# Kernel optimization log

Measured on AMD Instinct MI355X. Metric: run time of the kernel, lower is better.

The kernel has to match this reference:

```python
import jax, jax.numpy as jnp
import numpy as np

K = 20
EPS = 1e-5
SLOPE = 0.2


def _knn_idx(x, k):
    # x: [B, C, N] -> idx [B, N, k] of nearest neighbors by squared L2
    sq = jnp.sum(x * x, axis=1)                      # [B, N]
    inner = jnp.einsum('bcn,bcm->bnm', x, x)         # [B, N, N]
    neg_dist = 2.0 * inner - sq[:, :, None] - sq[:, None, :]
    return jax.lax.top_k(neg_dist, k)[1]             # [B, N, k]


def _edge_block(x, W, gamma, beta, k):
    # x: [B, C, N]; W: [O, 2C]; returns [B, O, N]
    idx = _knn_idx(x, k)
    xt = jnp.transpose(x, (0, 2, 1))                 # [B, N, C]
    nb = jax.vmap(lambda t, i: t[i])(xt, idx)        # [B, N, k, C] gather
    ctr = xt[:, :, None, :]
    edge = jnp.concatenate(
        [nb - ctr, jnp.broadcast_to(ctr, nb.shape)], axis=-1)  # [B, N, k, 2C]
    y = jnp.einsum('bnkc,oc->bonk', edge, W)         # 1x1 conv
    # BatchNorm2d (training mode: batch stats over B,N,k per channel)
    m = jnp.mean(y, axis=(0, 2, 3), keepdims=True)
    v = jnp.var(y, axis=(0, 2, 3), keepdims=True)
    y = (y - m) * jax.lax.rsqrt(v + EPS)
    y = y * gamma[None, :, None, None] + beta[None, :, None, None]
    y = jnp.where(y >= 0, y, SLOPE * y)              # LeakyReLU(0.2)
    return jnp.max(y, axis=-1)                       # max over k neighbors


def setup_inputs() -> dict:
    key = jax.random.key(0)
    ks = jax.random.split(key, 8)
    B, N = 8, 2048
    x = jax.random.normal(ks[0], (B, N, 3), dtype=jnp.float32)
    W1 = jax.random.normal(ks[1], (64, 6), dtype=jnp.float32) * 0.2
    W2 = jax.random.normal(ks[2], (128, 128), dtype=jnp.float32) * 0.08
    W3 = jax.random.normal(ks[3], (256, 256), dtype=jnp.float32) * 0.06
    g1, b1 = jnp.ones((64,), jnp.float32), jnp.zeros((64,), jnp.float32)
    g2, b2 = jnp.ones((128,), jnp.float32), jnp.zeros((128,), jnp.float32)
    g3, b3 = jnp.ones((256,), jnp.float32), jnp.zeros((256,), jnp.float32)
    L1 = jax.random.normal(ks[4], (1024, 448), dtype=jnp.float32) * 0.04
    L2 = jax.random.normal(ks[5], (2500, 1024), dtype=jnp.float32) * 0.03
    return {"x": x, "W1": W1, "g1": g1, "b1": b1, "W2": W2, "g2": g2,
            "b2": b2, "W3": W3, "g3": g3, "b3": b3, "L1": L1, "L2": L2}


def reference(x, W1, g1, b1, W2, g2, b2, W3, g3, b3, L1, L2):
    xT = jnp.transpose(x, (0, 2, 1))                 # [B, 3, N]
    x1 = _edge_block(xT, W1, g1, b1, K)              # [B, 64, N]
    x2 = _edge_block(x1, W2, g2, b2, K)              # [B, 128, N]
    x3 = _edge_block(x2, W3, g3, b3, K)              # [B, 256, N]
    feat = jnp.concatenate([x1, x2, x3], axis=1)     # [B, 448, N]
    pooled = jnp.max(feat, axis=-1)                  # adaptive_max_pool1d(1)
    h = pooled @ L1.T
    h = jnp.where(h >= 0, h, SLOPE * h)              # LeakyReLU(0.2)
    # dropout is identity in eval mode
    return h @ L2.T                                  # [B, 2500]
```

## Files before the change

### kernel.cpp

```cpp
#include <hip/hip_runtime.h>
#include <hip/hip_bf16.h>
#include <float.h>

#define K_NN 20
#define EPS 1e-5f
#define SLOPE 0.2f
constexpr int Bsz = 8;
constexpr int Npts = 2048;
constexpr int NQ = 8;
constexpr int BN = Bsz * Npts;

typedef __attribute__((ext_vector_type(8))) short short8v;
typedef __attribute__((ext_vector_type(4))) float f32x4;

__device__ __forceinline__ float dot4(float4 a, float4 b) {
  return a.x*b.x + a.y*b.y + a.z*b.z + a.w*b.w;
}
__device__ __forceinline__ unsigned encf(float f) {
  unsigned u = __float_as_uint(f);
  return (u & 0x80000000u) ? ~u : (u | 0x80000000u);
}
__device__ __forceinline__ float decf(unsigned e) {
  unsigned u = (e & 0x80000000u) ? (e & 0x7fffffffu) : ~e;
  return __uint_as_float(u);
}
__device__ __forceinline__ unsigned short f2bf(float x) {
  unsigned u = __float_as_uint(x);
  unsigned r = (u + 0x7fffu + ((u >> 16) & 1u)) >> 16;
  return (unsigned short)r;
}
__device__ __forceinline__ float bf2f(unsigned short h) {
  return __uint_as_float((unsigned)h << 16);
}
__device__ __forceinline__ f32x4 mfma16(short8v a, short8v b, f32x4 c) {
  return __builtin_amdgcn_mfma_f32_16x16x32_bf16(a, b, c, 0, 0, 0);
}

template<int C>
__global__ __launch_bounds__(256) void sq_kernel(const float* __restrict__ xt,
                                                 float* __restrict__ sq) {
  int p = blockIdx.x * 256 + threadIdx.x;
  if (p >= BN) return;
  const float* r = xt + (size_t)p * C;
  float s = 0.f;
  if constexpr (C % 4 == 0) {
    for (int c4 = 0; c4 < C / 4; ++c4) { float4 v = *(const float4*)(r + c4 * 4); s += dot4(v, v); }
  } else {
    #pragma unroll
    for (int c = 0; c < C; ++c) { float v = r[c]; s += v * v; }
  }
  sq[p] = s;
}

template<int C, int MT>
__global__ __launch_bounds__(256) void knn_part(const float* __restrict__ xt,
    const float* __restrict__ sq, float* __restrict__ pval, int* __restrict__ pidx) {
  constexpr int MQ = Npts / NQ;
  __shared__ __align__(16) float chk[MT][C];
  __shared__ float csq[MT];
  const int t = threadIdx.x, w = t >> 6, l = t & 63;
  const int rowblk = blockIdx.x / NQ;
  const int q = blockIdx.x - rowblk * NQ;
  const int p0 = rowblk * 256;
  const int b = p0 / Npts;
  const int myrow = p0 + w * 64 + l;

  float cr[C];
  #pragma unroll
  for (int c = 0; c < C; ++c) cr[c] = xt[(size_t)myrow * C + c];
  const float sqn = sq[myrow];

  float vals[K_NN]; int ids[K_NN];
  #pragma unroll
  for (int i = 0; i < K_NN; ++i) { vals[i] = -FLT_MAX; ids[i] = 0; }

  const int mbase = q * MQ;
  for (int m0 = mbase; m0 < mbase + MQ; m0 += MT) {
    __syncthreads();
    const float* s2 = xt + ((size_t)b * Npts + m0) * C;
    for (int e = t; e < MT * C; e += 256) chk[e / C][e - (e / C) * C] = s2[e];
    for (int e = t; e < MT; e += 256) csq[e] = sq[b * Npts + m0 + e];
    __syncthreads();
    for (int j = 0; j < MT; ++j) {
      float dt = 0.f;
      #pragma unroll
      for (int c = 0; c < C; ++c) dt += cr[c] * chk[j][c];
      float nd = 2.f * dt - sqn - csq[j];
      if (nd > vals[K_NN - 1]) {
        vals[K_NN - 1] = nd; ids[K_NN - 1] = m0 + j;
        #pragma unroll
        for (int i = K_NN - 1; i >= 1; --i) {
          if (vals[i] > vals[i - 1]) {
            float tv = vals[i]; vals[i] = vals[i-1]; vals[i-1] = tv;
            int ti = ids[i]; ids[i] = ids[i-1]; ids[i-1] = ti;
          }
        }
      }
    }
  }
  size_t base = ((size_t)q * BN + myrow) * K_NN;
  #pragma unroll
  for (int i = 0; i < K_NN; ++i) { pval[base + i] = vals[i]; pidx[base + i] = ids[i]; }
}

__global__ __launch_bounds__(256) void knn_merge(const float* __restrict__ pval,
    const int* __restrict__ pidx, int* __restrict__ idxout) {
  int p = blockIdx.x * 256 + threadIdx.x;
  if (p >= BN) return;
  float vals[K_NN]; int ids[K_NN];
  size_t base = (size_t)p * K_NN;
  #pragma unroll
  for (int i = 0; i < K_NN; ++i) { vals[i] = pval[base + i]; ids[i] = pidx[base + i]; }
  for (int q = 1; q < NQ; ++q) {
    size_t b2 = ((size_t)q * BN + p) * K_NN;
    #pragma unroll
    for (int i = 0; i < K_NN; ++i) {
      float v = pval[b2 + i];
      if (v <= vals[K_NN - 1]) break;
      int m = pidx[b2 + i];
      vals[K_NN - 1] = v; ids[K_NN - 1] = m;
      #pragma unroll
      for (int r = K_NN - 1; r >= 1; --r) {
        if (vals[r] > vals[r - 1]) {
          float tv = vals[r]; vals[r] = vals[r-1]; vals[r-1] = tv;
          int ti = ids[r]; ids[r] = ids[r-1]; ids[r-1] = ti;
        }
      }
    }
  }
  int* op = idxout + (size_t)p * K_NN;
  #pragma unroll
  for (int i = 0; i < K_NN; ++i) op[i] = ids[i];
}

template<int C>
__global__ __launch_bounds__(256) void knn_fused(
    const unsigned short* __restrict__ xh, const unsigned short* __restrict__ xl,
    const float* __restrict__ sq, int* __restrict__ idxout) {
  constexpr int KS = C / 32;
  constexpr int TPW = Npts / 64 / 4;
  __shared__ float dist[4][64][17];
  __shared__ float svv[4][16][K_NN];
  __shared__ int   sii[4][16][K_NN];
  const int b = blockIdx.x >> 7, qt = blockIdx.x & 127;
  const int q0 = qt * 16;
  const int t = threadIdx.x, wv = t >> 6, l = t & 63, l15 = l & 15, grp = l >> 4;
  const unsigned short* xbh = xh + (size_t)b * Npts * C;
  const unsigned short* xbl = xl + (size_t)b * Npts * C;
  const float* sqb = sq + b * Npts;
  const int qi = q0 + l15;

  short8v bh[KS], bl[KS];
  #pragma unroll
  for (int ks = 0; ks < KS; ++ks) {
    const size_t a = (size_t)qi * C + ks * 32 + grp * 8;
    bh[ks] = *(const short8v*)(xbh + a);
    bl[ks] = *(const short8v*)(xbl + a);
  }
  const float sqn = sqb[qi];

  float vals[K_NN]; int ids[K_NN];
  #pragma unroll
  for (int i = 0; i < K_NN; ++i) { vals[i] = -FLT_MAX; ids[i] = 0; }

  #pragma unroll 1
  for (int ti = 0; ti < TPW; ++ti) {
    const int m0 = (wv * TPW + ti) * 64;
    f32x4 acc[4];
    #pragma unroll
    for (int rt = 0; rt < 4; ++rt) acc[rt] = (f32x4){0.f, 0.f, 0.f, 0.f};
    #pragma unroll
    for (int ks = 0; ks < KS; ++ks) {
      #pragma unroll
      for (int rt = 0; rt < 4; ++rt) {
        const size_t aoff = (size_t)(m0 + rt * 16 + l15) * C + ks * 32 + grp * 8;
        const short8v a_h = *(const short8v*)(xbh + aoff);
        const short8v a_l = *(const short8v*)(xbl + aoff);
        acc[rt] = mfma16(a_h, bh[ks], acc[rt]);
        acc[rt] = mfma16(a_l, bh[ks], acc[rt]);
        acc[rt] = mfma16(a_h, bl[ks], acc[rt]);
      }
    }
    #pragma unroll
    for (int rt = 0; rt < 4; ++rt) {
      const int cb = m0 + rt * 16 + grp * 4;
      const float4 s4 = *(const float4*)(sqb + cb);
      const float sv[4] = {s4.x, s4.y, s4.z, s4.w};
      #pragma unroll
      for (int r = 0; r < 4; ++r) {
        const int cand = cb + r;
        float v = 2.f * acc[rt][r] - sqn - sv[r];
        if (cand == qi) v = 0.f;
        dist[wv][rt * 16 + grp * 4 + r][l15] = v;
      }
    }
    asm volatile("s_waitcnt lgkmcnt(0)" ::: "memory");
    __builtin_amdgcn_sched_barrier(0);
    #pragma unroll 1
    for (int j = 0; j < 16; ++j) {
      const float v = dist[wv][grp * 16 + j][l15];
      if (v > vals[K_NN - 1]) {
        const int cand = m0 + grp * 16 + j;
        vals[K_NN - 1] = v; ids[K_NN - 1] = cand;
        #pragma unroll
        for (int i = K_NN - 1; i >= 1; --i) {
          if (vals[i] > vals[i - 1]) {
            float tv = vals[i]; vals[i] = vals[i-1]; vals[i-1] = tv;
            int ti2 = ids[i]; ids[i] = ids[i-1]; ids[i-1] = ti2;
          }
        }
      }
    }
  }

  #pragma unroll
  for (int s2 = 1; s2 < 4; ++s2) {
    float ov[K_NN]; int oi[K_NN];
    #pragma unroll
    for (int i = 0; i < K_NN; ++i) {
      ov[i] = __shfl(vals[i], s2 * 16 + l15);
      oi[i] = __shfl(ids[i],  s2 * 16 + l15);
    }
    if (grp == 0) {
      #pragma unroll
      for (int i = 0; i < K_NN; ++i) {
        const float v = ov[i];
        if (v <= vals[K_NN - 1]) break;
        vals[K_NN - 1] = v; ids[K_NN - 1] = oi[i];
        #pragma unroll
        for (int r = K_NN - 1; r >= 1; --r) {
          if (vals[r] > vals[r - 1]) {
            float tv = vals[r]; vals[r] = vals[r-1]; vals[r-1] = tv;
            int ti2 = ids[r]; ids[r] = ids[r-1]; ids[r-1] = ti2;
          }
        }
      }
    }
  }
  if (grp == 0) {
    #pragma unroll
    for (int i = 0; i < K_NN; ++i) { svv[wv][l15][i] = vals[i]; sii[wv][l15][i] = ids[i]; }
  }
  __syncthreads();
  if (t < 16) {
    #pragma unroll
    for (int s2 = 1; s2 < 4; ++s2) {
      #pragma unroll
      for (int i = 0; i < K_NN; ++i) {
        const float v = svv[s2][t][i];
        if (v <= vals[K_NN - 1]) break;
        vals[K_NN - 1] = v; ids[K_NN - 1] = sii[s2][t][i];
        #pragma unroll
        for (int r = K_NN - 1; r >= 1; --r) {
          if (vals[r] > vals[r - 1]) {
            float tv = vals[r]; vals[r] = vals[r-1]; vals[r-1] = tv;
            int ti2 = ids[r]; ids[r] = ids[r-1]; ids[r-1] = ti2;
          }
        }
      }
    }
    int* op = idxout + ((size_t)(b * Npts + q0 + t)) * K_NN;
    #pragma unroll
    for (int i = 0; i < K_NN; ++i) op[i] = ids[i];
  }
}

template<int C, int O>
__global__ __launch_bounds__(256) void prep_w(const float* __restrict__ W,
    unsigned short* __restrict__ wh, unsigned short* __restrict__ wl) {
  int i = blockIdx.x * 256 + threadIdx.x;
  if (i >= 2 * O * C) return;
  int j = i / C, c = i - j * C;
  float v = (j < O) ? W[(size_t)j * 2 * C + c]
                    : (W[(size_t)(j - O) * 2 * C + C + c] - W[(size_t)(j - O) * 2 * C + c]);
  unsigned short h = f2bf(v);
  wh[i] = h; wl[i] = f2bf(v - bf2f(h));
}

template<int C, int N2>
__global__ __launch_bounds__(256) void zgemm(
    const unsigned short* __restrict__ xh, const unsigned short* __restrict__ xl,
    const unsigned short* __restrict__ wh, const unsigned short* __restrict__ wl,
    float* __restrict__ Z, int r0) {
  constexpr int KS = C / 32;
  constexpr int CB = N2 / 64;
  const int nb = blockIdx.x / CB, cb = blockIdx.x - nb * CB;
  const int ln0 = nb * 64;
  const int t = threadIdx.x, l = t & 63, wv = t >> 6, l15 = l & 15, grp = l >> 4;
  const int col = cb * 64 + wv * 16 + l15;
  f32x4 acc[4];
  #pragma unroll
  for (int rt = 0; rt < 4; ++rt) acc[rt] = (f32x4){0.f, 0.f, 0.f, 0.f};
  #pragma unroll
  for (int ks = 0; ks < KS; ++ks) {
    const int krd = ks * 32 + grp * 8;
    const short8v bh = *(const short8v*)(wh + (size_t)col * C + krd);
    const short8v bl = *(const short8v*)(wl + (size_t)col * C + krd);
    #pragma unroll
    for (int rt = 0; rt < 4; ++rt) {
      const size_t arow = (size_t)(r0 + ln0 + rt * 16 + l15) * C + krd;
      const short8v a_h = *(const short8v*)(xh + arow);
      const short8v a_l = *(const short8v*)(xl + arow);
      acc[rt] = mfma16(a_h, bh, acc[rt]);
      acc[rt] = mfma16(a_l, bh, acc[rt]);
      acc[rt] = mfma16(a_h, bl, acc[rt]);
    }
  }
  #pragma unroll
  for (int rt = 0; rt < 4; ++rt)
    #pragma unroll
    for (int r = 0; r < 4; ++r)
      Z[(size_t)(ln0 + rt * 16 + grp * 4 + r) * N2 + col] = acc[rt][r];
}

template<int O, int NPP>
__global__ __launch_bounds__(256) void nbr_reduce(
    const float* __restrict__ Z, const int* __restrict__ idx,
    float* __restrict__ mx, float* __restrict__ mn,
    float* __restrict__ psum, float* __restrict__ psq, int r0) {
  constexpr int PPB = 256 / O;
  constexpr int O2 = 2 * O;
  const int t = threadIdx.x;
  const int o = t % O;
  const int sub = t / O;
  float ls = 0.f, lq = 0.f;
  for (int it = 0; it < NPP / PPB; ++it) {
    const int p = r0 + blockIdx.x * NPP + it * PPB + sub;
    const int bbase = (p >> 11) << 11;
    const int* ip = idx + (size_t)p * K_NN;
    const float base = Z[(size_t)(p - r0) * O2 + O + o];
    float vmx = -FLT_MAX, vmn = FLT_MAX;
    #pragma unroll
    for (int k = 0; k < K_NN; ++k) {
      const int nbrow = bbase + ip[k] - r0;
      const float y = Z[(size_t)nbrow * O2 + o] + base;
      ls += y; lq = fmaf(y, y, lq);
      vmx = fmaxf(vmx, y); vmn = fminf(vmn, y);
    }
    mx[(size_t)p * O + o] = vmx;
    mn[(size_t)p * O + o] = vmn;
  }
  if constexpr (PPB > 1) {
    __shared__ float s1[256], s2[256];
    s1[t] = ls; s2[t] = lq;
    __syncthreads();
    if (sub == 0) {
      psum[(size_t)blockIdx.x * O + o] = ls + s1[t + O];
      psq [(size_t)blockIdx.x * O + o] = lq + s2[t + O];
    }
  } else {
    psum[(size_t)blockIdx.x * O + o] = ls;
    psq [(size_t)blockIdx.x * O + o] = lq;
  }
}

template<int C, int O, int G, int NPG, int CPT>
__global__ __launch_bounds__(256) void edge_kernel(const float* __restrict__ xt,
    const int* __restrict__ idx, const float* __restrict__ W,
    float* __restrict__ mx, float* __restrict__ mn,
    float* __restrict__ psum, float* __restrict__ psq) {
  constexpr int WP = O / (64 * CPT);
  constexpr int TPB = 64 * WP * NPG;
  constexpr int PPG = G / NPG;
  static_assert(TPB == 256, "block must be 256 threads");
  __shared__ __align__(16) float pts[G][K_NN + 1][C];
  __shared__ int ids[G][K_NN + 1];
  __shared__ float shps[NPG][O];
  __shared__ float shpq[NPG][O];
  const int t = threadIdx.x;
  const int p0 = blockIdx.x * G;
  const int b = p0 / Npts;

  for (int e = t; e < G * (K_NN + 1); e += TPB) {
    int g = e / (K_NN + 1), j = e - g * (K_NN + 1);
    ids[g][j] = (j == 0) ? (p0 + g) : (b * Npts + idx[(size_t)(p0 + g) * K_NN + (j - 1)]);
  }
  __syncthreads();
  for (int e = t; e < G * (K_NN + 1) * C; e += TPB) {
    int g = e / ((K_NN + 1) * C), rem = e - g * ((K_NN + 1) * C);
    int j = rem / C, c = rem - j * C;
    pts[g][j][c] = xt[(size_t)ids[g][j] * C + c];
  }
  __syncthreads();

  const int w = t >> 6, l = t & 63;
  const int pg = w / WP, wp = w - pg * WP;
  const int o0 = wp * 64 + l;
  float ls0 = 0.f, lq0 = 0.f;

  for (int it = 0; it < PPG; ++it) {
    const int g = pg * PPG + it;
    float yk0[K_NN];
    float u0 = 0.f, v0 = 0.f;
    #pragma unroll
    for (int k = 0; k < K_NN; ++k) yk0[k] = 0.f;
    const float* W0 = W + (size_t)o0 * (2 * C);
    #pragma unroll
    for (int c = 0; c < C; ++c) {
      const float wl = W0[c], whv = W0[C + c], ccv = pts[g][0][c];
      u0 += wl * ccv; v0 += whv * ccv;
      #pragma unroll
      for (int k = 0; k < K_NN; ++k) yk0[k] += wl * pts[g][k + 1][c];
    }
    const int n = p0 + g - b * Npts;
    const size_t obase = ((size_t)b * Npts + n) * O;
    const float base = v0 - u0;
    float vmx = -FLT_MAX, vmn = FLT_MAX;
    #pragma unroll
    for (int k = 0; k < K_NN; ++k) {
      float y = yk0[k] + base;
      ls0 += y; lq0 += y * y;
      vmx = fmaxf(vmx, y); vmn = fminf(vmn, y);
    }
    mx[obase + o0] = vmx; mn[obase + o0] = vmn;
  }

  shps[pg][o0] = ls0; shpq[pg][o0] = lq0;
  __syncthreads();
  if (t < O) {
    float s = 0.f, qq = 0.f;
    #pragma unroll
    for (int i = 0; i < NPG; ++i) { s += shps[i][t]; qq += shpq[i][t]; }
    psum[(size_t)blockIdx.x * O + t] = s;
    psq [(size_t)blockIdx.x * O + t] = qq;
  }
}

template<int O, int NBLK>
__global__ __launch_bounds__(256) void stats_part(const float* __restrict__ psum,
    const float* __restrict__ psq, double* __restrict__ pp, double* __restrict__ pq) {
  constexpr int NS = 16;
  constexpr int SL = NBLK / NS;
  const int l = threadIdx.x & 63, w = threadIdx.x >> 6;
  const int os = blockIdx.x % (O / 64), sl = blockIdx.x / (O / 64);
  const int o = os * 64 + l;
  double s = 0.0, ss = 0.0;
  for (int i = sl * SL + w; i < (sl + 1) * SL; i += 4) {
    s  += (double)psum[(size_t)i * O + o];
    ss += (double)psq [(size_t)i * O + o];
  }
  __shared__ double sh[2][4][64];
  sh[0][w][l] = s; sh[1][w][l] = ss;
  __syncthreads();
  if (w == 0) {
    s  = sh[0][0][l] + sh[0][1][l] + sh[0][2][l] + sh[0][3][l];
    ss = sh[1][0][l] + sh[1][1][l] + sh[1][2][l] + sh[1][3][l];
    pp[(size_t)sl * O + o] = s;
    pq[(size_t)sl * O + o] = ss;
  }
}

template<int O>
__global__ __launch_bounds__(64) void stats_final(const double* __restrict__ pp,
    const double* __restrict__ pq,
    const float* __restrict__ gamma, const float* __restrict__ beta,
    float* __restrict__ scale, float* __restrict__ bias) {
  const int o = blockIdx.x * 64 + threadIdx.x;
  double s = 0.0, ss = 0.0;
  #pragma unroll
  for (int sl = 0; sl < 16; ++sl) { s += pp[(size_t)sl * O + o]; ss += pq[(size_t)sl * O + o]; }
  double cnt = (double)Bsz * Npts * K_NN;
  double m = s / cnt;
  double var = ss / cnt - m * m;
  float g = gamma[o];
  float sc = g * rsqrtf((float)var + EPS);
  scale[o] = sc;
  bias[o] = beta[o] - (float)m * sc;
}

__global__ __launch_bounds__(256) void reset_pool(unsigned* __restrict__ pooled) {
  int i = blockIdx.x * 256 + threadIdx.x;
  if (i < Bsz * 448) pooled[i] = 0u;
}

template<int O, int COFF, bool WNC>
__global__ __launch_bounds__(256) void apply_kernel(const float* __restrict__ mx,
    const float* __restrict__ mn, const float* __restrict__ scale,
    const float* __restrict__ bias, float* __restrict__ xnc,
    unsigned short* __restrict__ xh, unsigned short* __restrict__ xl,
    unsigned* __restrict__ pooled) {
  constexpr int OT = O / 64;
  constexpr int NCH = Npts / 256;
  const int bid = blockIdx.x;
  const int nchunk = bid % NCH;
  const int ot = (bid / NCH) % OT;
  const int b = bid / (NCH * OT);
  const int l = threadIdx.x & 63, w = threadIdx.x >> 6;
  const int o = ot * 64 + l;
  const float sc = scale[o], bs = bias[o];
  const bool pos = (sc >= 0.f);
  float vmax = -FLT_MAX;
  const int n0 = nchunk * 256;
  for (int i = 0; i < 64; ++i) {
    int n = n0 + w + i * 4;
    size_t ix = ((size_t)b * Npts + n) * O + o;
    float raw = pos ? mx[ix] : mn[ix];
    float y = raw * sc + bs;
    y = (y >= 0.f) ? y : SLOPE * y;
    if constexpr (WNC) {
      xnc[ix] = y;
      unsigned short h = f2bf(y);
      xh[ix] = h;
      xl[ix] = f2bf(y - bf2f(h));
    }
    vmax = fmaxf(vmax, y);
  }
  __shared__ float sh[4][64];
  sh[w][l] = vmax;
  __syncthreads();
  if (w == 0) {
    float m = fmaxf(fmaxf(sh[0][l], sh[1][l]), fmaxf(sh[2][l], sh[3][l]));
    atomicMax(pooled + b * 448 + COFF + o, encf(m));
  }
}

template<int CIN, bool LRELU, bool DECODE>
__global__ __launch_bounds__(64) void fc_kernel(const void* __restrict__ inv,
    const float* __restrict__ Wt, float* __restrict__ out, int JO) {
  int j = blockIdx.x;
  const float* wr = Wt + (size_t)j * CIN;
  float acc[Bsz];
  #pragma unroll
  for (int b = 0; b < Bsz; ++b) acc[b] = 0.f;
  for (int c = threadIdx.x; c < CIN; c += 64) {
    float wv = wr[c];
    #pragma unroll
    for (int b = 0; b < Bsz; ++b) {
      float x;
      if constexpr (DECODE) x = decf(((const unsigned*)inv)[b * CIN + c]);
      else                  x = ((const float*)inv)[b * CIN + c];
      acc[b] += x * wv;
    }
  }
  #pragma unroll
  for (int b = 0; b < Bsz; ++b) {
    float v = acc[b];
    #pragma unroll
    for (int w = 32; w > 0; w >>= 1) v += __shfl_down(v, w);
    if (threadIdx.x == 0) {
      if (LRELU) v = (v >= 0.f) ? v : SLOPE * v;
      out[b * JO + j] = v;
    }
  }
}

extern "C" void kernel_launch(void* const* d_in, const int* in_sizes, int n_in,
                              void* d_out, int out_size, void* d_ws, size_t ws_size,
                              hipStream_t stream) {
  const float* x   = (const float*)d_in[0];
  const float* W1  = (const float*)d_in[1];
  const float* g1  = (const float*)d_in[2];
  const float* b1  = (const float*)d_in[3];
  const float* W2  = (const float*)d_in[4];
  const float* g2  = (const float*)d_in[5];
  const float* b2  = (const float*)d_in[6];
  const float* W3  = (const float*)d_in[7];
  const float* g3  = (const float*)d_in[8];
  const float* b3  = (const float*)d_in[9];
  const float* L1  = (const float*)d_in[10];
  const float* L2  = (const float*)d_in[11];
  float* out = (float*)d_out;

  float* ws = (float*)d_ws;
  size_t off = 0;
  float* sq    = ws + off; off += BN;
  int*   idxb  = (int*)(ws + off); off += (size_t)BN * K_NN;
  float* mx    = ws + off; off += (size_t)BN * 256;
  float* mn    = ws + off; off += (size_t)BN * 256;
  float* Z     = ws + off; off += (size_t)BN * 256;
  float* psum  = ws + off; off += (size_t)2048 * 256;
  float* psq   = ws + off; off += (size_t)2048 * 256;
  off = (off + 1) & ~(size_t)1;
  double* pp   = (double*)(ws + off); off += 16 * 256 * 2;
  double* pq   = (double*)(ws + off); off += 16 * 256 * 2;
  float* scale = ws + off; off += 256;
  float* bias  = ws + off; off += 256;
  float* x1nc  = ws + off; off += (size_t)BN * 64;
  float* x2nc  = ws + off; off += (size_t)BN * 128;
  unsigned short* xh1 = (unsigned short*)(ws + off); off += (size_t)BN * 64 / 2;
  unsigned short* xl1 = (unsigned short*)(ws + off); off += (size_t)BN * 64 / 2;
  unsigned short* xh2 = (unsigned short*)(ws + off); off += (size_t)BN * 128 / 2;
  unsigned short* xl2 = (unsigned short*)(ws + off); off += (size_t)BN * 128 / 2;
  unsigned* pooled = (unsigned*)(ws + off); off += Bsz * 448;
  float* h     = ws + off; off += Bsz * 1024;
  unsigned short* wch2 = (unsigned short*)(ws + off); off += 256 * 64 / 2;
  unsigned short* wcl2 = (unsigned short*)(ws + off); off += 256 * 64 / 2;
  unsigned short* wch3 = (unsigned short*)(ws + off); off += 512 * 128 / 2;
  unsigned short* wcl3 = (unsigned short*)(ws + off); off += 512 * 128 / 2;
  float* pval = mx;
  int*   pidx = (int*)mn;

  reset_pool<<<14, 256, 0, stream>>>(pooled);
  prep_w<64, 128><<<(2 * 128 * 64 + 255) / 256, 256, 0, stream>>>(W2, wch2, wcl2);
  prep_w<128, 256><<<(2 * 256 * 128 + 255) / 256, 256, 0, stream>>>(W3, wch3, wcl3);

  sq_kernel<3><<<64, 256, 0, stream>>>(x, sq);
  knn_part<3, 64><<<(BN / 256) * NQ, 256, 0, stream>>>(x, sq, pval, pidx);
  knn_merge<<<64, 256, 0, stream>>>(pval, pidx, idxb);
  edge_kernel<3, 64, 16, 4, 1><<<BN / 16, 256, 0, stream>>>(x, idxb, W1, mx, mn, psum, psq);
  stats_part<64, 1024><<<16, 256, 0, stream>>>(psum, psq, pp, pq);
  stats_final<64><<<1, 64, 0, stream>>>(pp, pq, g1, b1, scale, bias);
  apply_kernel<64, 0, true><<<64, 256, 0, stream>>>(mx, mn, scale, bias, x1nc, xh1, xl1, pooled);

  sq_kernel<64><<<64, 256, 0, stream>>>(x1nc, sq);
  knn_fused<64><<<Bsz * 128, 256, 0, stream>>>(xh1, xl1, sq, idxb);
  zgemm<64, 256><<<(BN / 64) * 4, 256, 0, stream>>>(xh1, xl1, wch2, wcl2, Z, 0);
  nbr_reduce<128, 16><<<BN / 16, 256, 0, stream>>>(Z, idxb, mx, mn, psum, psq, 0);
  stats_part<128, 1024><<<32, 256, 0, stream>>>(psum, psq, pp, pq);
  stats_final<128><<<2, 64, 0, stream>>>(pp, pq, g2, b2, scale, bias);
  apply_kernel<128, 64, true><<<128, 256, 0, stream>>>(mx, mn, scale, bias, x2nc, xh2, xl2, pooled);

  sq_kernel<128><<<64, 256, 0, stream>>>(x2nc, sq);
  knn_fused<128><<<Bsz * 128, 256, 0, stream>>>(xh2, xl2, sq, idxb);
  for (int pass = 0; pass < 2; ++pass) {
    const int r0 = pass * (BN / 2);
    zgemm<128, 512><<<(BN / 2 / 64) * 8, 256, 0, stream>>>(xh2, xl2, wch3, wcl3, Z, r0);
    nbr_reduce<256, 8><<<BN / 2 / 8, 256, 0, stream>>>(Z, idxb, mx, mn,
        psum + (size_t)pass * 1024 * 256, psq + (size_t)pass * 1024 * 256, r0);
  }
  stats_part<256, 2048><<<64, 256, 0, stream>>>(psum, psq, pp, pq);
  stats_final<256><<<4, 64, 0, stream>>>(pp, pq, g3, b3, scale, bias);
  apply_kernel<256, 192, false><<<256, 256, 0, stream>>>(mx, mn, scale, bias, nullptr, nullptr, nullptr, pooled);

  fc_kernel<448, true, true><<<1024, 64, 0, stream>>>(pooled, L1, h, 1024);
  fc_kernel<1024, false, false><<<2500, 64, 0, stream>>>(h, L2, out, 2500);
}
```

Baseline: 1.009 ms.

## Split fused kNN candidate range across two blocks and merge partial top-k lists

The fused MFMA kNN kernel now splits each query tile's 2048 candidates into two halves handled by separate blocks, doubling the grid to give the GPU more parallel work. Each block writes a partial top-20 list to scratch, and a templated merge kernel combines the two halves into the final indices. Shared memory for distances and merge buffers is aliased to reduce LDS use, which adds a barrier, and the selection loop gets partial unrolling. The cost is an extra kernel launch per layer plus the scratch writes and reads of partial results.

```diff
diff --git a/kernel.cpp b/kernel.cpp
--- a/kernel.cpp
+++ b/kernel.cpp
@@ -103,6 +103,7 @@
   for (int i = 0; i < K_NN; ++i) { pval[base + i] = vals[i]; pidx[base + i] = ids[i]; }
 }
 
+template<int NQM>
 __global__ __launch_bounds__(256) void knn_merge(const float* __restrict__ pval,
     const int* __restrict__ pidx, int* __restrict__ idxout) {
   int p = blockIdx.x * 256 + threadIdx.x;
@@ -111,7 +112,8 @@
   size_t base = (size_t)p * K_NN;
   #pragma unroll
   for (int i = 0; i < K_NN; ++i) { vals[i] = pval[base + i]; ids[i] = pidx[base + i]; }
-  for (int q = 1; q < NQ; ++q) {
+  #pragma unroll
+  for (int q = 1; q < NQM; ++q) {
     size_t b2 = ((size_t)q * BN + p) * K_NN;
     #pragma unroll
     for (int i = 0; i < K_NN; ++i) {
@@ -136,13 +138,17 @@
 template<int C>
 __global__ __launch_bounds__(256) void knn_fused(
     const unsigned short* __restrict__ xh, const unsigned short* __restrict__ xl,
-    const float* __restrict__ sq, int* __restrict__ idxout) {
+    const float* __restrict__ sq, float* __restrict__ pval, int* __restrict__ pidx) {
   constexpr int KS = C / 32;
-  constexpr int TPW = Npts / 64 / 4;
-  __shared__ float dist[4][64][17];
-  __shared__ float svv[4][16][K_NN];
-  __shared__ int   sii[4][16][K_NN];
-  const int b = blockIdx.x >> 7, qt = blockIdx.x & 127;
+  constexpr int TPW = 4;
+  __shared__ __align__(16) char smem[4 * 64 * 17 * 4];
+  float (*dist)[64][17] = (float(*)[64][17])smem;
+  float (*svv)[16][K_NN] = (float(*)[16][K_NN])smem;
+  int   (*sii)[16][K_NN] = (int(*)[16][K_NN])(smem + 4 * 16 * K_NN * 4);
+  const int bid = blockIdx.x;
+  const int b = bid >> 8;
+  const int rem = bid & 255;
+  const int qt = rem >> 1, h = rem & 1;
   const int q0 = qt * 16;
   const int t = threadIdx.x, wv = t >> 6, l = t & 63, l15 = l & 15, grp = l >> 4;
   const unsigned short* xbh = xh + (size_t)b * Npts * C;
@@ -165,7 +171,7 @@
 
   #pragma unroll 1
   for (int ti = 0; ti < TPW; ++ti) {
-    const int m0 = (wv * TPW + ti) * 64;
+    const int m0 = h * 1024 + (wv * TPW + ti) * 64;
     f32x4 acc[4];
     #pragma unroll
     for (int rt = 0; rt < 4; ++rt) acc[rt] = (f32x4){0.f, 0.f, 0.f, 0.f};
@@ -196,7 +202,7 @@
     }
     asm volatile("s_waitcnt lgkmcnt(0)" ::: "memory");
     __builtin_amdgcn_sched_barrier(0);
-    #pragma unroll 1
+    #pragma unroll 4
     for (int j = 0; j < 16; ++j) {
       const float v = dist[wv][grp * 16 + j][l15];
       if (v > vals[K_NN - 1]) {
@@ -237,6 +243,7 @@
       }
     }
   }
+  __syncthreads();
   if (grp == 0) {
     #pragma unroll
     for (int i = 0; i < K_NN; ++i) { svv[wv][l15][i] = vals[i]; sii[wv][l15][i] = ids[i]; }
@@ -259,9 +266,9 @@
         }
       }
     }
-    int* op = idxout + ((size_t)(b * Npts + q0 + t)) * K_NN;
-    #pragma unroll
-    for (int i = 0; i < K_NN; ++i) op[i] = ids[i];
+    size_t base = ((size_t)h * BN + b * Npts + q0 + t) * K_NN;
+    #pragma unroll
+    for (int i = 0; i < K_NN; ++i) { pval[base + i] = vals[i]; pidx[base + i] = ids[i]; }
   }
 }
 
@@ -596,14 +603,15 @@
 
   sq_kernel<3><<<64, 256, 0, stream>>>(x, sq);
   knn_part<3, 64><<<(BN / 256) * NQ, 256, 0, stream>>>(x, sq, pval, pidx);
-  knn_merge<<<64, 256, 0, stream>>>(pval, pidx, idxb);
+  knn_merge<NQ><<<64, 256, 0, stream>>>(pval, pidx, idxb);
   edge_kernel<3, 64, 16, 4, 1><<<BN / 16, 256, 0, stream>>>(x, idxb, W1, mx, mn, psum, psq);
   stats_part<64, 1024><<<16, 256, 0, stream>>>(psum, psq, pp, pq);
   stats_final<64><<<1, 64, 0, stream>>>(pp, pq, g1, b1, scale, bias);
   apply_kernel<64, 0, true><<<64, 256, 0, stream>>>(mx, mn, scale, bias, x1nc, xh1, xl1, pooled);
 
   sq_kernel<64><<<64, 256, 0, stream>>>(x1nc, sq);
-  knn_fused<64><<<Bsz * 128, 256, 0, stream>>>(xh1, xl1, sq, idxb);
+  knn_fused<64><<<Bsz * 256, 256, 0, stream>>>(xh1, xl1, sq, pval, pidx);
+  knn_merge<2><<<64, 256, 0, stream>>>(pval, pidx, idxb);
   zgemm<64, 256><<<(BN / 64) * 4, 256, 0, stream>>>(xh1, xl1, wch2, wcl2, Z, 0);
   nbr_reduce<128, 16><<<BN / 16, 256, 0, stream>>>(Z, idxb, mx, mn, psum, psq, 0);
   stats_part<128, 1024><<<32, 256, 0, stream>>>(psum, psq, pp, pq);
@@ -611,7 +619,8 @@
   apply_kernel<128, 64, true><<<128, 256, 0, stream>>>(mx, mn, scale, bias, x2nc, xh2, xl2, pooled);
 
   sq_kernel<128><<<64, 256, 0, stream>>>(x2nc, sq);
-  knn_fused<128><<<Bsz * 128, 256, 0, stream>>>(xh2, xl2, sq, idxb);
+  knn_fused<128><<<Bsz * 256, 256, 0, stream>>>(xh2, xl2, sq, pval, pidx);
+  knn_merge<2><<<64, 256, 0, stream>>>(pval, pidx, idxb);
   for (int pass = 0; pass < 2; ++pass) {
     const int r0 = pass * (BN / 2);
     zgemm<128, 512><<<(BN / 2 / 64) * 8, 256, 0, stream>>>(xh2, xl2, wch3, wcl3, Z, r0);
```

Measured after the change: 1.028 ms. About the same (+1.9%).

## Co-schedule kNN and independent Z-GEMM blocks in one launch

Applied to the files above, without the earlier changes.

Merges the kNN kernel and the Z projection GEMM, which both depend only on the layer input, into one launch whose block index range picks which body runs. kNN blocks (latency- and ALU-bound top-k) and MFMA GEMM blocks can then share the GPU at the same time, and one launch boundary per layer goes away. In exchange, the GEMM blocks now carry the shared-memory footprint of the kNN path, which can limit occupancy, and the layer-3 first-half GEMM is restructured to fit.

```diff
diff --git a/kernel.cpp b/kernel.cpp
--- a/kernel.cpp
+++ b/kernel.cpp
@@ -134,15 +134,13 @@
 }
 
 template<int C>
-__global__ __launch_bounds__(256) void knn_fused(
+__device__ __forceinline__ void knn_body(
     const unsigned short* __restrict__ xh, const unsigned short* __restrict__ xl,
-    const float* __restrict__ sq, int* __restrict__ idxout) {
+    const float* __restrict__ sq, int* __restrict__ idxout, int bid,
+    float (*dist)[64][17], float (*svv)[16][K_NN], int (*sii)[16][K_NN]) {
   constexpr int KS = C / 32;
   constexpr int TPW = Npts / 64 / 4;
-  __shared__ float dist[4][64][17];
-  __shared__ float svv[4][16][K_NN];
-  __shared__ int   sii[4][16][K_NN];
-  const int b = blockIdx.x >> 7, qt = blockIdx.x & 127;
+  const int b = bid >> 7, qt = bid & 127;
   const int q0 = qt * 16;
   const int t = threadIdx.x, wv = t >> 6, l = t & 63, l15 = l & 15, grp = l >> 4;
   const unsigned short* xbh = xh + (size_t)b * Npts * C;
@@ -265,6 +263,66 @@
   }
 }
 
+template<int C, int N2>
+__device__ __forceinline__ void zgemm_body(
+    const unsigned short* __restrict__ xh, const unsigned short* __restrict__ xl,
+    const unsigned short* __restrict__ wh, const unsigned short* __restrict__ wl,
+    float* __restrict__ Z, int r0, int bid) {
+  constexpr int KS = C / 32;
+  constexpr int CB = N2 / 64;
+  const int nb = bid / CB, cb = bid - nb * CB;
+  const int ln0 = nb * 64;
+  const int t = threadIdx.x, l = t & 63, wv = t >> 6, l15 = l & 15, grp = l >> 4;
+  const int col = cb * 64 + wv * 16 + l15;
+  f32x4 acc[4];
+  #pragma unroll
+  for (int rt = 0; rt < 4; ++rt) acc[rt] = (f32x4){0.f, 0.f, 0.f, 0.f};
+  #pragma unroll
+  for (int ks = 0; ks < KS; ++ks) {
+    const int krd = ks * 32 + grp * 8;
+    const short8v bh = *(const short8v*)(wh + (size_t)col * C + krd);
+    const short8v bl = *(const short8v*)(wl + (size_t)col * C + krd);
+    #pragma unroll
+    for (int rt = 0; rt < 4; ++rt) {
+      const size_t arow = (size_t)(r0 + ln0 + rt * 16 + l15) * C + krd;
+      const short8v a_h = *(const short8v*)(xh + arow);
+      const short8v a_l = *(const short8v*)(xl + arow);
+      acc[rt] = mfma16(a_h, bh, acc[rt]);
+      acc[rt] = mfma16(a_l, bh, acc[rt]);
+      acc[rt] = mfma16(a_h, bl, acc[rt]);
+    }
+  }
+  #pragma unroll
+  for (int rt = 0; rt < 4; ++rt)
+    #pragma unroll
+    for (int r = 0; r < 4; ++r)
+      Z[(size_t)(ln0 + rt * 16 + grp * 4 + r) * N2 + col] = acc[rt][r];
+}
+
+template<int C, int N2, int KNNB>
+__global__ __launch_bounds__(256) void knn_zgemm(
+    const unsigned short* __restrict__ xh, const unsigned short* __restrict__ xl,
+    const float* __restrict__ sq, int* __restrict__ idxout,
+    const unsigned short* __restrict__ wh, const unsigned short* __restrict__ wl,
+    float* __restrict__ Z, int r0) {
+  __shared__ float dist[4][64][17];
+  __shared__ float svv[4][16][K_NN];
+  __shared__ int   sii[4][16][K_NN];
+  if ((int)blockIdx.x < KNNB) {
+    knn_body<C>(xh, xl, sq, idxout, blockIdx.x, dist, svv, sii);
+  } else {
+    zgemm_body<C, N2>(xh, xl, wh, wl, Z, r0, blockIdx.x - KNNB);
+  }
+}
+
+template<int C, int N2>
+__global__ __launch_bounds__(256) void zgemm(
+    const unsigned short* __restrict__ xh, const unsigned short* __restrict__ xl,
+    const unsigned short* __restrict__ wh, const unsigned short* __restrict__ wl,
+    float* __restrict__ Z, int r0) {
+  zgemm_body<C, N2>(xh, xl, wh, wl, Z, r0, blockIdx.x);
+}
+
 template<int C, int O>
 __global__ __launch_bounds__(256) void prep_w(const float* __restrict__ W,
     unsigned short* __restrict__ wh, unsigned short* __restrict__ wl) {
@@ -275,42 +333,6 @@
                     : (W[(size_t)(j - O) * 2 * C + C + c] - W[(size_t)(j - O) * 2 * C + c]);
   unsigned short h = f2bf(v);
   wh[i] = h; wl[i] = f2bf(v - bf2f(h));
-}
-
-template<int C, int N2>
-__global__ __launch_bounds__(256) void zgemm(
-    const unsigned short* __restrict__ xh, const unsigned short* __restrict__ xl,
-    const unsigned short* __restrict__ wh, const unsigned short* __restrict__ wl,
-    float* __restrict__ Z, int r0) {
-  constexpr int KS = C / 32;
-  constexpr int CB = N2 / 64;
-  const int nb = blockIdx.x / CB, cb = blockIdx.x - nb * CB;
-  const int ln0 = nb * 64;
-  const int t = threadIdx.x, l = t & 63, wv = t >> 6, l15 = l & 15, grp = l >> 4;
-  const int col = cb * 64 + wv * 16 + l15;
-  f32x4 acc[4];
-  #pragma unroll
-  for (int rt = 0; rt < 4; ++rt) acc[rt] = (f32x4){0.f, 0.f, 0.f, 0.f};
-  #pragma unroll
-  for (int ks = 0; ks < KS; ++ks) {
-    const int krd = ks * 32 + grp * 8;
-    const short8v bh = *(const short8v*)(wh + (size_t)col * C + krd);
-    const short8v bl = *(const short8v*)(wl + (size_t)col * C + krd);
-    #pragma unroll
-    for (int rt = 0; rt < 4; ++rt) {
-      const size_t arow = (size_t)(r0 + ln0 + rt * 16 + l15) * C + krd;
-      const short8v a_h = *(const short8v*)(xh + arow);
-      const short8v a_l = *(const short8v*)(xl + arow);
-      acc[rt] = mfma16(a_h, bh, acc[rt]);
-      acc[rt] = mfma16(a_l, bh, acc[rt]);
-      acc[rt] = mfma16(a_h, bl, acc[rt]);
-    }
-  }
-  #pragma unroll
-  for (int rt = 0; rt < 4; ++rt)
-    #pragma unroll
-    for (int r = 0; r < 4; ++r)
-      Z[(size_t)(ln0 + rt * 16 + grp * 4 + r) * N2 + col] = acc[rt][r];
 }
 
 template<int O, int NPP>
@@ -603,21 +625,20 @@
   apply_kernel<64, 0, true><<<64, 256, 0, stream>>>(mx, mn, scale, bias, x1nc, xh1, xl1, pooled);
 
   sq_kernel<64><<<64, 256, 0, stream>>>(x1nc, sq);
-  knn_fused<64><<<Bsz * 128, 256, 0, stream>>>(xh1, xl1, sq, idxb);
-  zgemm<64, 256><<<(BN / 64) * 4, 256, 0, stream>>>(xh1, xl1, wch2, wcl2, Z, 0);
+  knn_zgemm<64, 256, Bsz * 128><<<Bsz * 128 + (BN / 64) * 4, 256, 0, stream>>>(
+      xh1, xl1, sq, idxb, wch2, wcl2, Z, 0);
   nbr_reduce<128, 16><<<BN / 16, 256, 0, stream>>>(Z, idxb, mx, mn, psum, psq, 0);
   stats_part<128, 1024><<<32, 256, 0, stream>>>(psum, psq, pp, pq);
   stats_final<128><<<2, 64, 0, stream>>>(pp, pq, g2, b2, scale, bias);
   apply_kernel<128, 64, true><<<128, 256, 0, stream>>>(mx, mn, scale, bias, x2nc, xh2, xl2, pooled);
 
   sq_kernel<128><<<64, 256, 0, stream>>>(x2nc, sq);
-  knn_fused<128><<<Bsz * 128, 256, 0, stream>>>(xh2, xl2, sq, idxb);
-  for (int pass = 0; pass < 2; ++pass) {
-    const int r0 = pass * (BN / 2);
-    zgemm<128, 512><<<(BN / 2 / 64) * 8, 256, 0, stream>>>(xh2, xl2, wch3, wcl3, Z, r0);
-    nbr_reduce<256, 8><<<BN / 2 / 8, 256, 0, stream>>>(Z, idxb, mx, mn,
-        psum + (size_t)pass * 1024 * 256, psq + (size_t)pass * 1024 * 256, r0);
-  }
+  knn_zgemm<128, 512, Bsz * 128><<<Bsz * 128 + (BN / 2 / 64) * 8, 256, 0, stream>>>(
+      xh2, xl2, sq, idxb, wch3, wcl3, Z, 0);
+  nbr_reduce<256, 8><<<BN / 2 / 8, 256, 0, stream>>>(Z, idxb, mx, mn, psum, psq, 0);
+  zgemm<128, 512><<<(BN / 2 / 64) * 8, 256, 0, stream>>>(xh2, xl2, wch3, wcl3, Z, BN / 2);
+  nbr_reduce<256, 8><<<BN / 2 / 8, 256, 0, stream>>>(Z, idxb, mx, mn,
+      psum + (size_t)1024 * 256, psq + (size_t)1024 * 256, BN / 2);
   stats_part<256, 2048><<<64, 256, 0, stream>>>(psum, psq, pp, pq);
   stats_final<256><<<4, 64, 0, stream>>>(pp, pq, g3, b3, scale, bias);
   apply_kernel<256, 192, false><<<256, 256, 0, stream>>>(mx, mn, scale, bias, nullptr, nullptr, nullptr, pooled);
```

Measured after the change: 3.049 ms. 3.02x slower.
